# Optimization experiments

Hardware: AMD Instinct MI355X
Metric: run time of the kernel (lower is better)

Reference implementation:

```python
import jax, jax.numpy as jnp
import numpy as np

EPS = 1e-12  # F.normalize default eps


def _unfold(x, k, pad, stride):
    # torch F.unfold: [B,C,H,W] -> [B, C*k*k, L], features ordered (c, kh, kw), L row-major.
    B, C, H, W = x.shape
    xp = jnp.pad(x, ((0, 0), (0, 0), (pad, pad), (pad, pad)))
    Ho = (H + 2 * pad - k) // stride + 1
    Wo = (W + 2 * pad - k) // stride + 1
    r = (jnp.arange(Ho) * stride)[:, None] + jnp.arange(k)[None, :]  # [Ho,k]
    c = (jnp.arange(Wo) * stride)[:, None] + jnp.arange(k)[None, :]  # [Wo,k]
    p = xp[:, :, r[:, None, :, None], c[None, :, None, :]]  # [B,C,Ho,Wo,k,k]
    return p.transpose(0, 1, 4, 5, 2, 3).reshape(B, C * k * k, Ho * Wo)


def _fold(p, out_hw, k, pad, stride):
    # torch F.fold: overlap-add inverse of _unfold.
    B, CKK, L = p.shape
    C = CKK // (k * k)
    H, W = out_hw
    Ho = (H + 2 * pad - k) // stride + 1
    Wo = (W + 2 * pad - k) // stride + 1
    p = p.reshape(B, C, k, k, Ho, Wo).transpose(0, 1, 4, 5, 2, 3)  # [B,C,Ho,Wo,k,k]
    r = (jnp.arange(Ho) * stride)[:, None] + jnp.arange(k)[None, :]
    c = (jnp.arange(Wo) * stride)[:, None] + jnp.arange(k)[None, :]
    out = jnp.zeros((B, C, H + 2 * pad, W + 2 * pad), p.dtype)
    out = out.at[:, :, r[:, None, :, None], c[None, :, None, :]].add(p)
    return out[:, :, pad:pad + H, pad:pad + W]


def _l2n(x, axis):
    n = jnp.sqrt(jnp.sum(x * x, axis=axis, keepdims=True))
    return x / jnp.maximum(n, EPS)


def setup_inputs() -> dict:
    key = jax.random.key(0)
    ks = jax.random.split(key, 11)
    B, H, W = 1, 32, 32
    f = jnp.float32
    return {
        'lrsr_lv3': jax.random.normal(ks[0], (B, 256, H, W), f),
        'refsr_lv1': jax.random.normal(ks[1], (B, 64, 4 * H, 4 * W), f),
        'refsr_lv2': jax.random.normal(ks[2], (B, 128, 2 * H, 2 * W), f),
        'refsr_lv3': jax.random.normal(ks[3], (B, 256, H, W), f),
        'ref_lv1': jax.random.normal(ks[4], (B, 64, 4 * H, 4 * W), f),
        'ref_lv2': jax.random.normal(ks[5], (B, 128, 2 * H, 2 * W), f),
        'ref_lv3': jax.random.normal(ks[6], (B, 256, H, W), f),
        'W1': jax.random.normal(ks[7], (2304, 1152), f) * 0.02,
        'b1': jax.random.normal(ks[8], (2304,), f) * 0.02,
        'W2': jax.random.normal(ks[9], (2304, 576), f) * 0.02,
        'b2': jax.random.normal(ks[10], (2304,), f) * 0.02,
    }


def reference(lrsr_lv3, refsr_lv1, refsr_lv2, refsr_lv3, ref_lv1, ref_lv2, ref_lv3, W1, b1, W2, b2):
    B, _, H, W = lrsr_lv3.shape
    lr3 = _unfold(lrsr_lv3, 3, 1, 1)                       # [B, 2304, N]
    r3 = _unfold(refsr_lv3, 3, 1, 1).transpose(0, 2, 1)    # [B, N3, 2304]
    r2 = _unfold(refsr_lv2, 3, 1, 1).transpose(0, 2, 1) @ W1.T + b1  # [B, N2, 2304]
    r1 = _unfold(refsr_lv1, 3, 1, 1).transpose(0, 2, 1) @ W2.T + b2  # [B, N1, 2304]
    r3 = _l2n(r3, 2); r2 = _l2n(r2, 2); r1 = _l2n(r1, 2)
    lr3 = _l2n(lr3, 1)
    R3 = jnp.einsum('bnd,bdm->bnm', r3, lr3)  # [B, N3, N]
    R2 = jnp.einsum('bnd,bdm->bnm', r2, lr3)  # [B, N2, N]
    R1 = jnp.einsum('bnd,bdm->bnm', r1, lr3)  # [B, N1, N]
    R3_star = jnp.max(R3, axis=1); R3_arg = jnp.argmax(R3, axis=1)
    R2_star = jnp.max(R2, axis=1)
    R1_star = jnp.max(R1, axis=1)
    ref3u = _unfold(ref_lv3, 3, 1, 1)
    ref2u = _unfold(ref_lv2, 6, 2, 2)
    ref1u = _unfold(ref_lv1, 12, 4, 4)
    idx = R3_arg[:, None, :]  # [B,1,N] broadcast over feature dim
    T3u = jnp.take_along_axis(ref3u, idx, axis=2)
    T2u = jnp.take_along_axis(ref2u, idx, axis=2)
    T1u = jnp.take_along_axis(ref1u, idx, axis=2)
    T_lv3 = _fold(T3u, (H, W), 3, 1, 1) / 9.0
    T_lv2 = _fold(T2u, (2 * H, 2 * W), 6, 2, 2) / 9.0
    T_lv1 = _fold(T1u, (4 * H, 4 * W), 12, 4, 4) / 9.0
    S_3 = R3_star.reshape(B, 1, H, W)
    S_2 = R2_star.reshape(B, 1, H, W)
    S_1 = R1_star.reshape(B, 1, H, W)
    return (S_1, S_2, S_3, T_lv3, T_lv2, T_lv1)
```

## Files before the change

### kernel.cpp

```cpp
#include <hip/hip_runtime.h>

typedef short bf8 __attribute__((ext_vector_type(8)));
typedef float f32x4 __attribute__((ext_vector_type(4)));

static __device__ __forceinline__ unsigned short f2bf(float f) {
  unsigned u = __float_as_uint(f);
  unsigned r = u + 0x7FFFu + ((u >> 16) & 1u);
  return (unsigned short)(r >> 16);
}
static __device__ __forceinline__ float bf2f(unsigned short h) {
  return __uint_as_float(((unsigned)h) << 16);
}
static __device__ __forceinline__ unsigned fkey(float f) {
  unsigned u = __float_as_uint(f);
  return (u & 0x80000000u) ? ~u : (u | 0x80000000u);
}
static __device__ __forceinline__ float kdec(unsigned k) {
  unsigned u = (k & 0x80000000u) ? (k & 0x7FFFFFFFu) : ~k;
  return __uint_as_float(u);
}
static __device__ __forceinline__ int xcdswz(int h, int nwg) {
  int q = nwg >> 3, r = nwg & 7;
  int xcd = h & 7, w = h >> 3;
  return (xcd < r ? xcd * (q + 1) : r * (q + 1) + (xcd - r) * q) + w;
}
static __device__ __forceinline__ int xcdbal(int h, int nwg, int nb0) {
  int xcd = h & 7, w = h >> 3;
  int qa = nb0 >> 3, qb = (nwg - nb0) >> 3;
  return (w < qa) ? (xcd * qa + w) : (nb0 + xcd * qb + (w - qa));
}

static __device__ __forceinline__ void gload_lds16(const unsigned short* g, unsigned short* l) {
  __builtin_amdgcn_global_load_lds((const __attribute__((address_space(1))) void*)g,
                                   (__attribute__((address_space(3))) void*)l, 16, 0, 0);
}

static __device__ __forceinline__ float uf3(const float* __restrict__ src, int lgS, int d, int m) {
  const int S = 1 << lgS;
  int cc = d / 9;
  int r9 = d - cc * 9;
  int ki = r9 / 3;
  int kj = r9 - ki * 3;
  int i = (m >> lgS) + ki - 1;
  int j = (m & (S - 1)) + kj - 1;
  if ((unsigned)i >= (unsigned)S || (unsigned)j >= (unsigned)S) return 0.f;
  return src[((size_t)cc << (2 * lgS)) + ((size_t)i << lgS) + j];
}

__global__ __launch_bounds__(256) void k_prepA(const float* __restrict__ lrsr3, const float* __restrict__ rsr3,
                                               const float* __restrict__ rsr2, const float* __restrict__ rsr1,
                                               const float* __restrict__ W1, const float* __restrict__ W2,
                                               const float* __restrict__ b1, const float* __restrict__ b2,
                                               float* __restrict__ sclr, float* __restrict__ scu3,
                                               float* __restrict__ bl2, float* __restrict__ bl1,
                                               float* __restrict__ G2,
                                               float* __restrict__ rsr2t, float* __restrict__ rsr1t,
                                               unsigned short* __restrict__ lr3nbT,
                                               unsigned short* __restrict__ W1t, unsigned short* __restrict__ W2t) {
  const int blk = blockIdx.x;
  const int tid = threadIdx.x;
  if (blk < 2048) {
    __shared__ float r0[256], r1[256], r2[256];
    const bool lr = blk < 1024;
    const int m = blk & 1023;
    const float* src = lr ? lrsr3 : rsr3;
    float s = 0.f, d1 = 0.f, d2 = 0.f;
    for (int d = tid; d < 2304; d += 256) {
      float v = uf3(src, 5, d, m);
      s += v * v; d1 += b1[d] * v; d2 += b2[d] * v;
    }
    r0[tid] = s; r1[tid] = d1; r2[tid] = d2;
    __syncthreads();
    for (int o = 128; o > 0; o >>= 1) {
      if (tid < o) { r0[tid] += r0[tid + o]; r1[tid] += r1[tid + o]; r2[tid] += r2[tid + o]; }
      __syncthreads();
    }
    if (tid == 0) {
      float sc = 1.f / fmaxf(sqrtf(r0[0]), 1e-12f);
      if (lr) { sclr[m] = sc; bl2[m] = r1[0] * sc; bl1[m] = r2[0] * sc; }
      else    { scu3[m] = sc; }
    }
  } else if (blk < 3072) {
    __shared__ float As[16][32], Bs[16][32];
    const int px = blk - 2048;
    const int m0 = (px >> 5) * 32, n0 = (px & 31) * 32;
    const int tx = tid & 15, ty = tid >> 4;
    float acc[2][2] = {};
    for (int kb = 0; kb < 256; kb += 16) {
      __syncthreads();
      {
        int kk = tid >> 5, mm = tid & 31;
        As[kk][mm] = lrsr3[(size_t)(kb + kk) * 1024 + m0 + mm];
        Bs[kk][mm] = rsr3[(size_t)(kb + kk) * 1024 + n0 + mm];
        int e2 = tid + 256; int kk2 = e2 >> 5, mm2 = e2 & 31;
        As[kk2][mm2] = lrsr3[(size_t)(kb + kk2) * 1024 + m0 + mm2];
        Bs[kk2][mm2] = rsr3[(size_t)(kb + kk2) * 1024 + n0 + mm2];
      }
      __syncthreads();
#pragma unroll
      for (int kk = 0; kk < 16; ++kk) {
        float a0 = As[kk][ty * 2], a1 = As[kk][ty * 2 + 1];
        float b0 = Bs[kk][tx * 2], b1v = Bs[kk][tx * 2 + 1];
        acc[0][0] = fmaf(a0, b0, acc[0][0]); acc[0][1] = fmaf(a0, b1v, acc[0][1]);
        acc[1][0] = fmaf(a1, b0, acc[1][0]); acc[1][1] = fmaf(a1, b1v, acc[1][1]);
      }
    }
#pragma unroll
    for (int i = 0; i < 2; ++i)
#pragma unroll
      for (int jj = 0; jj < 2; ++jj)
        G2[(size_t)(m0 + ty * 2 + i) * 1024 + (n0 + tx * 2 + jj)] = acc[i][jj];
  } else if (blk < 3200) {
    __shared__ float Tt[64][65];
    const int idx = blk - 3072;
    const int ct = idx & 1, st = idx >> 1;
#pragma unroll
    for (int i = 0; i < 16; ++i) {
      int id = tid + i * 256;
      int r = id >> 6, c = id & 63;
      Tt[r][c] = rsr2[(size_t)(ct * 64 + r) * 4096 + st * 64 + c];
    }
    __syncthreads();
#pragma unroll
    for (int i = 0; i < 16; ++i) {
      int id = tid + i * 256;
      int cc2 = id >> 6, rr = id & 63;
      rsr2t[(size_t)(st * 64 + cc2) * 128 + ct * 64 + rr] = Tt[rr][cc2];
    }
  } else if (blk < 3456) {
    __shared__ float Tt[64][65];
    const int st = blk - 3200;
#pragma unroll
    for (int i = 0; i < 16; ++i) {
      int id = tid + i * 256;
      int r = id >> 6, c = id & 63;
      Tt[r][c] = rsr1[(size_t)r * 16384 + st * 64 + c];
    }
    __syncthreads();
#pragma unroll
    for (int i = 0; i < 16; ++i) {
      int id = tid + i * 256;
      int cc2 = id >> 6, rr = id & 63;
      rsr1t[(size_t)(st * 64 + cc2) * 64 + rr] = Tt[rr][cc2];
    }
  } else if (blk < 4608) {
    int id8 = (blk - 3456) * 256 + tid;
    int m = id8 / 288, c0 = (id8 - m * 288) * 8;
    bf8 v;
#pragma unroll
    for (int e = 0; e < 8; ++e) v[e] = (short)f2bf(uf3(lrsr3, 5, c0 + e, m));
    *(bf8*)(lr3nbT + (size_t)m * 2304 + c0) = v;
  } else {
    __shared__ unsigned short Ls[64][65];
    int idx = blk - 4608;
    int xx = idx % 27, yy = idx / 27;
    const float* W; unsigned short* Wt; int Cw, c0;
    if (xx < 18) { W = W1; Wt = W1t; Cw = 1152; c0 = xx * 64; }
    else         { W = W2; Wt = W2t; Cw = 576;  c0 = (xx - 18) * 64; }
    const int Cch = Cw / 9;
    const int d0 = yy * 64;
#pragma unroll
    for (int i = 0; i < 16; ++i) {
      int id = tid + i * 256;
      int r = id >> 6, c = id & 63;
      Ls[r][c] = f2bf(W[(size_t)(d0 + r) * Cw + c0 + c]);
    }
    __syncthreads();
#pragma unroll
    for (int i = 0; i < 16; ++i) {
      int id = tid + i * 256;
      int cc = id >> 6, rr = id & 63;
      int c = c0 + cc;
      Wt[(size_t)((c % 9) * Cch + c / 9) * 2304 + d0 + rr] = Ls[rr][cc];
    }
  }
}

struct Job {
  const unsigned short* Alo;
  const unsigned short* Ahi;
  const unsigned short* Bt;
  unsigned short* Clo;
  unsigned short* Chi;
  const float* bl;
  const float* bw;
  const float* bbp;
  const float* rowscale;
  float* pnsq;
  float* pbwd;
  float* cmax;
  int Msplit, N, K, nbx, Mtot, npart, which;
};

template <int EPI, int NBUF>
static __device__ __forceinline__ void gemm_body(const Job& j0, const Job& j1, int nb0, int bid) {
  __shared__ __align__(16) unsigned short As[NBUF][128 * 64];
  __shared__ __align__(16) unsigned short Bs[NBUF][128 * 64];
  __shared__ unsigned colkey[128];
  __shared__ float ninvL[128];

  const bool first = (bid < nb0);
  const Job j = first ? j0 : j1;
  const int local = bid - (first ? 0 : nb0);
  const int by = local / j.nbx;
  const int bx = local - by * j.nbx;
  const int m0 = by * 128, n0 = bx * 128;
  const int K = j.K, N = j.N;

  const unsigned short* Abase = (m0 < j.Msplit)
      ? j.Alo + (size_t)m0 * K
      : j.Ahi + (size_t)(m0 - j.Msplit) * K;

  const int tid = threadIdx.x;
  const int l = tid & 63;
  const int w = tid >> 6;
  const int wr = w >> 1, wc = w & 1;
  if (EPI == 2) {
    if (tid < 128) {
      colkey[tid] = 0u;
      const int r = m0 + tid;
      float nsq = 0.f, bwd = 0.f;
      for (int p = 0; p < j.npart; ++p) {
        nsq += j.pnsq[(size_t)p * j.Mtot + r];
        bwd += j.pbwd[(size_t)p * j.Mtot + r];
      }
      float tq = nsq + 2.f * bwd + j.bbp[j.which];
      ninvL[tid] = 1.f / fmaxf(sqrtf(fmaxf(tq, 0.f)), 1e-12f);
    }
  }

  f32x4 acc[4][4] = {};

  const int srow = w * 32;
  const int lrow = l >> 3;
  const int gcol = ((l & 7) ^ lrow) * 8;
  const int mr = l & 15;
  const int kg = l >> 4;

  const int nt = K >> 6;
  const int snap_kb = n0 + wc * 64;
  unsigned short snap[4][4][4];

  auto stage = [&](int buf, int kb) {
#pragma unroll
    for (int i = 0; i < 4; ++i) {
      int r = srow + i * 8;
      gload_lds16(Abase + (size_t)(r + lrow) * K + kb + gcol, &As[buf][r * 64]);
      gload_lds16(j.Bt + (size_t)(n0 + r + lrow) * K + kb + gcol, &Bs[buf][r * 64]);
    }
  };
  auto compute_tile = [&](int cur) {
#pragma unroll
    for (int ks = 0; ks < 2; ++ks) {
      bf8 af[4], bv[4];
#pragma unroll
      for (int mi = 0; mi < 4; ++mi) {
        const int row = wr * 64 + mi * 16 + mr;
        af[mi] = *(const bf8*)&As[cur][row * 64 + (((ks * 4 + kg) ^ (row & 7)) * 8)];
      }
#pragma unroll
      for (int ni = 0; ni < 4; ++ni) {
        const int row = wc * 64 + ni * 16 + mr;
        bv[ni] = *(const bf8*)&Bs[cur][row * 64 + (((ks * 4 + kg) ^ (row & 7)) * 8)];
      }
      __builtin_amdgcn_s_setprio(1);
#pragma unroll
      for (int mi = 0; mi < 4; ++mi)
#pragma unroll
        for (int ni = 0; ni < 4; ++ni)
          acc[mi][ni] = __builtin_amdgcn_mfma_f32_16x16x32_bf16(af[mi], bv[ni], acc[mi][ni], 0, 0, 0);
      __builtin_amdgcn_s_setprio(0);
    }
  };
  auto do_snap = [&](int cur) {
#pragma unroll
    for (int mi = 0; mi < 4; ++mi)
#pragma unroll
      for (int e = 0; e < 4; ++e) {
        const int row = wr * 64 + mi * 16 + kg * 4 + e;
#pragma unroll
        for (int ni = 0; ni < 4; ++ni) {
          const int slot = ni * 2 + (mr >> 3);
          snap[mi][ni][e] = As[cur][row * 64 + ((slot ^ (row & 7)) * 8) + (mr & 7)];
        }
      }
  };

  if constexpr (NBUF == 1) {
    for (int t = 0; t < nt; ++t) {
      if (t) __syncthreads();
      stage(0, t << 6);
      __syncthreads();
      compute_tile(0);
      if (EPI == 1 && (t << 6) == snap_kb) do_snap(0);
    }
  } else {
    auto waitv = [&](int Wt) {
      if (Wt >= 2)      asm volatile("s_waitcnt vmcnt(16)\ns_barrier" ::: "memory");
      else if (Wt == 1) asm volatile("s_waitcnt vmcnt(8)\ns_barrier" ::: "memory");
      else              asm volatile("s_waitcnt vmcnt(0)\ns_barrier" ::: "memory");
    };
#pragma unroll
    for (int p = 0; p < NBUF; ++p) if (p < nt) stage(p, p << 6);
    { int inflight = (NBUF < nt ? NBUF : nt); waitv(inflight - 1); }
    int cur = 0;
    for (int t = 0; t < nt; ++t) {
      compute_tile(cur);
      if (EPI == 1 && (t << 6) == snap_kb) do_snap(cur);
      if (t + 1 < nt) {
        asm volatile("s_waitcnt lgkmcnt(0)\ns_barrier" ::: "memory");
        if (t + NBUF < nt) stage(cur, (t + NBUF) << 6);
        const int im = (nt - 1 < t + NBUF) ? (nt - 1) : (t + NBUF);
        waitv(im - (t + 1));
        cur = (cur + 1 == NBUF) ? 0 : cur + 1;
      }
    }
  }

  const int lr0 = wr * 64;
  const int lc0 = wc * 64;
  if (EPI == 0) {
    const bool hi = (m0 >= j.Msplit);
    unsigned short* Cbase = hi ? j.Chi + (size_t)(m0 - j.Msplit) * N
                               : j.Clo + (size_t)m0 * N;
    float rs[4][4];
#pragma unroll
    for (int mi = 0; mi < 4; ++mi)
#pragma unroll
      for (int e = 0; e < 4; ++e)
        rs[mi][e] = hi ? j.rowscale[m0 - j.Msplit + lr0 + mi * 16 + kg * 4 + e] : 1.f;
#pragma unroll
    for (int mi = 0; mi < 4; ++mi)
#pragma unroll
      for (int ni = 0; ni < 4; ++ni)
#pragma unroll
        for (int e = 0; e < 4; ++e)
          Cbase[(size_t)(lr0 + mi * 16 + kg * 4 + e) * (size_t)N + (n0 + lc0 + ni * 16 + mr)] =
              f2bf(acc[mi][ni][e] * rs[mi][e]);
  } else if (EPI == 1) {
    float rp[4][4] = {};
    float bp[4][4] = {};
#pragma unroll
    for (int ni = 0; ni < 4; ++ni) {
      const float bwv = j.bw[n0 + lc0 + ni * 16 + mr];
#pragma unroll
      for (int mi = 0; mi < 4; ++mi)
#pragma unroll
        for (int e = 0; e < 4; ++e) {
          const float av = bf2f(snap[mi][ni][e]);
          rp[mi][e] += acc[mi][ni][e] * av;
          bp[mi][e] += bwv * av;
        }
    }
#pragma unroll
    for (int off = 1; off < 16; off <<= 1)
#pragma unroll
      for (int mi = 0; mi < 4; ++mi)
#pragma unroll
        for (int e = 0; e < 4; ++e) {
          rp[mi][e] += __shfl_xor(rp[mi][e], off);
          bp[mi][e] += __shfl_xor(bp[mi][e], off);
        }
    if (mr == 0) {
      const size_t slotbase = (size_t)(bx * 2 + wc) * j.Mtot;
#pragma unroll
      for (int mi = 0; mi < 4; ++mi)
#pragma unroll
        for (int e = 0; e < 4; ++e) {
          const int r = m0 + lr0 + mi * 16 + kg * 4 + e;
          j.pnsq[slotbase + r] = rp[mi][e];
          j.pbwd[slotbase + r] = bp[mi][e];
        }
    }
  } else {
    float nv[4][4];
#pragma unroll
    for (int mi = 0; mi < 4; ++mi)
#pragma unroll
      for (int e = 0; e < 4; ++e)
        nv[mi][e] = ninvL[lr0 + mi * 16 + kg * 4 + e];
#pragma unroll
    for (int ni = 0; ni < 4; ++ni) {
      float blv = j.bl[n0 + lc0 + ni * 16 + mr];
      float mx = -3.0e38f;
#pragma unroll
      for (int mi = 0; mi < 4; ++mi)
#pragma unroll
        for (int e = 0; e < 4; ++e) mx = fmaxf(mx, (acc[mi][ni][e] + blv) * nv[mi][e]);
      atomicMax(&colkey[lc0 + ni * 16 + mr], fkey(mx));
    }
    __syncthreads();
    if (tid < 128) j.cmax[(size_t)by * 1024 + n0 + tid] = kdec(colkey[tid]);
  }
}

__global__ __launch_bounds__(256) void k_prepBP(Job pa, Job pb, int nbP0,
                                                const float* __restrict__ rsr2t, const float* __restrict__ rsr1t,
                                                const float* __restrict__ W1, const float* __restrict__ W2,
                                                const float* __restrict__ b1, const float* __restrict__ b2,
                                                const float* __restrict__ sclr, const float* __restrict__ scu3,
                                                const float* __restrict__ G2,
                                                unsigned short* __restrict__ U2b, unsigned short* __restrict__ U1b,
                                                float* __restrict__ bw2, float* __restrict__ bw1,
                                                float* __restrict__ bb,
                                                float* __restrict__ s3, int* __restrict__ arg) {
  const int blk = blockIdx.x;
  const int tid = threadIdx.x;
  if (blk < 218) {
    gemm_body<0, 1>(pa, pb, nbP0, xcdswz(blk, 218));
  } else if (blk < 2522) {
    int id = (blk - 218) * 256 + tid;
    int t = id & 15, rest = id >> 4;
    int kk = rest % 9, n = rest / 9;
    int cc0 = t * 8;
    int ki = kk / 3, kj = kk - ki * 3;
    int sy = (n >> 6) + ki - 1, sx = (n & 63) + kj - 1;
    bf8 v;
    if ((unsigned)sy < 64u && (unsigned)sx < 64u) {
      const float* p = rsr2t + (size_t)(sy * 64 + sx) * 128 + cc0;
      f32x4 a = *(const f32x4*)p;
      f32x4 bq = *(const f32x4*)(p + 4);
#pragma unroll
      for (int e = 0; e < 4; ++e) { v[e] = (short)f2bf(a[e]); v[4 + e] = (short)f2bf(bq[e]); }
    } else {
#pragma unroll
      for (int e = 0; e < 8; ++e) v[e] = 0;
    }
    *(bf8*)(U2b + (size_t)n * 1152 + kk * 128 + cc0) = v;
  } else if (blk < 7642) {
    int id = (blk - 2522) * 256 + tid;
    int n = id / 80, rem = id - n * 80;
    int ks = rem >> 3, t = rem & 7;
    int cc0 = t * 8;
    bf8 v;
    if (ks == 9) {
#pragma unroll
      for (int e = 0; e < 8; ++e) v[e] = 0;
    } else {
      int ki = ks / 3, kj = ks - ki * 3;
      int sy = (n >> 7) + ki - 1, sx = (n & 127) + kj - 1;
      if ((unsigned)sy < 128u && (unsigned)sx < 128u) {
        const float* p = rsr1t + (size_t)(sy * 128 + sx) * 64 + cc0;
        f32x4 a = *(const f32x4*)p;
        f32x4 bq = *(const f32x4*)(p + 4);
#pragma unroll
        for (int e = 0; e < 4; ++e) { v[e] = (short)f2bf(a[e]); v[4 + e] = (short)f2bf(bq[e]); }
      } else {
#pragma unroll
        for (int e = 0; e < 8; ++e) v[e] = 0;
      }
    }
    *(bf8*)(U1b + (size_t)n * 640 + ks * 64 + cc0) = v;
  } else if (blk < 7722) {
    __shared__ float red[256];
    int idx = blk - 7642;
    int x = idx & 7, y = idx >> 3;
    if (y == 9) {
      if (x >= 2) return;
      const float* b = x ? b2 : b1;
      float s = 0.f;
      for (int d = tid; d < 2304; d += 256) s += b[d] * b[d];
      red[tid] = s; __syncthreads();
      for (int o = 128; o > 0; o >>= 1) { if (tid < o) red[tid] += red[tid + o]; __syncthreads(); }
      if (tid == 0) bb[x] = red[0];
      return;
    }
    const bool two = x < 5;
    const float* W = two ? W1 : W2;
    const float* b = two ? b1 : b2;
    float* bw = two ? bw2 : bw1;
    const int Cw = two ? 1152 : 576;
    int c = (two ? x : x - 5) * 256 + tid;
    if (c >= Cw) return;
    int d0 = y * 256;
    float s = 0.f;
    for (int d = d0; d < d0 + 256; ++d) s += b[d] * W[(size_t)d * Cw + c];
    atomicAdd(&bw[(c % 9) * (Cw / 9) + c / 9], s);
  } else {
    __shared__ float bv[256]; __shared__ int bidx[256];
    const int m = blk - 7722;
    const int mi = m >> 5, mj = m & 31;
    float best = -3.0e38f; int bi = 0;
    for (int n = tid; n < 1024; n += 256) {
      const int ni = n >> 5, nj = n & 31;
      float raw = 0.f;
#pragma unroll
      for (int dy = -1; dy <= 1; ++dy) {
#pragma unroll
        for (int dx = -1; dx <= 1; ++dx) {
          bool vm = ((unsigned)(mi + dy) < 32u) && ((unsigned)(mj + dx) < 32u);
          bool vn = ((unsigned)(ni + dy) < 32u) && ((unsigned)(nj + dx) < 32u);
          if (vm && vn) {
            int off = dy * 32 + dx;
            raw += G2[(size_t)(m + off) * 1024 + (n + off)];
          }
        }
      }
      float v = raw * scu3[n];
      if (v > best) { best = v; bi = n; }
    }
    bv[tid] = best; bidx[tid] = bi;
    __syncthreads();
    for (int o = 128; o > 0; o >>= 1) {
      if (tid < o) {
        float ov = bv[tid + o]; int oi = bidx[tid + o];
        if (ov > bv[tid] || (ov == bv[tid] && oi < bidx[tid])) { bv[tid] = ov; bidx[tid] = oi; }
      }
      __syncthreads();
    }
    if (tid == 0) { s3[m] = bv[0] * sclr[m]; arg[m] = bidx[0]; }
  }
}

__global__ __launch_bounds__(256) void k_gE1(Job a, Job b, int nb0) {
  gemm_body<1, 1>(a, b, nb0, xcdbal((int)blockIdx.x, (int)gridDim.x, nb0));
}
__global__ __launch_bounds__(256) void k_gE2(Job a, Job b, int nb0) {
  gemm_body<2, 1>(a, b, nb0, xcdbal((int)blockIdx.x, (int)gridDim.x, nb0));
}

__global__ __launch_bounds__(256) void k_tfold(const float* __restrict__ ref3, const float* __restrict__ ref2,
                                               const float* __restrict__ ref1, const int* __restrict__ arg,
                                               const float* __restrict__ cmax1, const float* __restrict__ cmax2,
                                               float* __restrict__ out) {
  const int bid = blockIdx.x;
  const int tid = threadIdx.x;
  if (bid < 256) {
    __shared__ float plane[1024];
    __shared__ int argL[1024];
    const int c = bid;
#pragma unroll
    for (int k = 0; k < 4; ++k) {
      plane[k * 256 + tid] = ref3[(size_t)c * 1024 + k * 256 + tid];
      argL[k * 256 + tid] = arg[k * 256 + tid];
    }
    __syncthreads();
#pragma unroll
    for (int k = 0; k < 4; ++k) {
      int px = k * 256 + tid;
      int y = px >> 5, x = px & 31;
      float s = 0.f;
#pragma unroll
      for (int di = -1; di <= 1; ++di) {
        int i = y + di;
        if ((unsigned)i >= 32u) continue;
#pragma unroll
        for (int dj = -1; dj <= 1; ++dj) {
          int jw = x + dj;
          if ((unsigned)jw >= 32u) continue;
          int n2 = argL[i * 32 + jw];
          int rr = (n2 >> 5) + y - i, cc = (n2 & 31) + x - jw;
          if ((unsigned)rr < 32u && (unsigned)cc < 32u) s += plane[rr * 32 + cc];
        }
      }
      out[3072 + (size_t)c * 1024 + px] = s * (1.f / 9.f);
    }
  } else if (bid < 1280) {
    __shared__ int argL[1024];
#pragma unroll
    for (int k = 0; k < 4; ++k) argL[k * 256 + tid] = arg[k * 256 + tid];
    __syncthreads();
    int id2 = (bid - 256) * 256 + tid;
    int q = id2 & 31, y = (id2 >> 5) & 63, c = id2 >> 11;
    int iy = y >> 1;
    float s0 = 0.f, s1 = 0.f;
#pragma unroll
    for (int di = -1; di <= 1; ++di) {
      int i = iy + di;
      if ((unsigned)i >= 32u) continue;
      int ry = y - 2 * i;
#pragma unroll
      for (int dj = -1; dj <= 1; ++dj) {
        int jw = q + dj;
        if ((unsigned)jw >= 32u) continue;
        int n2 = argL[i * 32 + jw];
        int rr = (n2 >> 5) * 2 + ry;
        int cb = (n2 & 31) * 2 + 2 * (q - jw);
        if ((unsigned)rr < 64u && (unsigned)cb < 63u) {
          const float* p = ref2 + (size_t)c * 4096 + rr * 64 + cb;
          s0 += p[0]; s1 += p[1];
        }
      }
    }
    float2 o; o.x = s0 * (1.f / 9.f); o.y = s1 * (1.f / 9.f);
    *(float2*)(out + 265216 + (size_t)c * 4096 + y * 64 + 2 * q) = o;
  } else if (bid < 2304) {
    __shared__ int argL[1024];
#pragma unroll
    for (int k = 0; k < 4; ++k) argL[k * 256 + tid] = arg[k * 256 + tid];
    __syncthreads();
    int id1 = (bid - 1280) * 256 + tid;
    int q = id1 & 31, y = (id1 >> 5) & 127, c = id1 >> 12;
    int iy = y >> 2;
    f32x4 s = {0.f, 0.f, 0.f, 0.f};
#pragma unroll
    for (int di = -1; di <= 1; ++di) {
      int i = iy + di;
      if ((unsigned)i >= 32u) continue;
      int ry = y - 4 * i;
#pragma unroll
      for (int dj = -1; dj <= 1; ++dj) {
        int jw = q + dj;
        if ((unsigned)jw >= 32u) continue;
        int n2 = argL[i * 32 + jw];
        int rr = (n2 >> 5) * 4 + ry;
        int cb = (n2 & 31) * 4 + 4 * (q - jw);
        if ((unsigned)rr < 128u && (unsigned)cb < 125u) {
          f32x4 v = *(const f32x4*)(ref1 + (size_t)c * 16384 + rr * 128 + cb);
          s += v;
        }
      }
    }
    s *= (1.f / 9.f);
    *(f32x4*)(out + 789504 + (size_t)c * 16384 + y * 128 + 4 * q) = s;
  } else {
    int t = (bid - 2304) * 256 + tid;
    if (t < 1024) {
      float mx = -3.0e38f;
      for (int rb = 0; rb < 128; ++rb) mx = fmaxf(mx, cmax1[rb * 1024 + t]);
      out[t] = mx;
    } else {
      int tt = t - 1024;
      float mx = -3.0e38f;
      for (int rb = 0; rb < 32; ++rb) mx = fmaxf(mx, cmax2[rb * 1024 + tt]);
      out[1024 + tt] = mx;
    }
  }
}

static constexpr size_t OFF_BW2     = 0;
static constexpr size_t OFF_BW1     = 4608;
static constexpr size_t ZERO_BYTES  = 7168;
static constexpr size_t OFF_BB      = 7168;
static constexpr size_t OFF_BL2     = 7424;
static constexpr size_t OFF_BL1     = 11520;
static constexpr size_t OFF_SCLR    = 15616;
static constexpr size_t OFF_SCU3    = 19712;
static constexpr size_t OFF_R3ARG   = 23808;
static constexpr size_t OFF_PNSQ2   = 27904;
static constexpr size_t OFF_PBWD2   = OFF_PNSQ2 + 294912;
static constexpr size_t OFF_PNSQ1   = OFF_PBWD2 + 294912;
static constexpr size_t OFF_PBWD1   = OFF_PNSQ1 + 655360;
static constexpr size_t OFF_CMAX2   = OFF_PBWD1 + 655360;
static constexpr size_t OFF_CMAX1   = OFF_CMAX2 + 131072;
static constexpr size_t OFF_LR3NBT  = OFF_CMAX1 + 524288;
static constexpr size_t OFF_U2B     = OFF_LR3NBT + 4718592;
static constexpr size_t OFF_U1B     = OFF_U2B    + 9437184;
static constexpr size_t OFF_W1T     = OFF_U1B    + 20971520;
static constexpr size_t OFF_W2T     = OFF_W1T    + 5308416;
static constexpr size_t OFF_A2      = OFF_W2T    + 2949120;
static constexpr size_t OFF_A1      = OFF_A2     + 2654208;
static constexpr size_t OFF_M2T     = OFF_A1     + 819200;
static constexpr size_t OFF_M1T     = OFF_M2T    + 2359296;
static constexpr size_t OFF_G2      = OFF_M1T    + 1310720;
static constexpr size_t OFF_R2T     = OFF_G2     + 4194304;
static constexpr size_t OFF_R1T     = OFF_R2T    + 2097152;

extern "C" void kernel_launch(void* const* d_in, const int* in_sizes, int n_in,
                              void* d_out, int out_size, void* d_ws, size_t ws_size,
                              hipStream_t stream) {
  (void)in_sizes; (void)n_in; (void)out_size; (void)ws_size;
  const float* lrsr3  = (const float*)d_in[0];
  const float* rsr1   = (const float*)d_in[1];
  const float* rsr2   = (const float*)d_in[2];
  const float* rsr3   = (const float*)d_in[3];
  const float* ref1   = (const float*)d_in[4];
  const float* ref2   = (const float*)d_in[5];
  const float* ref3   = (const float*)d_in[6];
  const float* W1     = (const float*)d_in[7];
  const float* b1     = (const float*)d_in[8];
  const float* W2     = (const float*)d_in[9];
  const float* b2     = (const float*)d_in[10];
  float* out = (float*)d_out;
  char* ws = (char*)d_ws;

  float*          bw2     = (float*)(ws + OFF_BW2);
  float*          bw1     = (float*)(ws + OFF_BW1);
  float*          bb      = (float*)(ws + OFF_BB);
  float*          bl2     = (float*)(ws + OFF_BL2);
  float*          bl1     = (float*)(ws + OFF_BL1);
  float*          sclr    = (float*)(ws + OFF_SCLR);
  float*          scu3    = (float*)(ws + OFF_SCU3);
  int*            R3arg   = (int*)(ws + OFF_R3ARG);
  float*          pnsq2   = (float*)(ws + OFF_PNSQ2);
  float*          pbwd2   = (float*)(ws + OFF_PBWD2);
  float*          pnsq1   = (float*)(ws + OFF_PNSQ1);
  float*          pbwd1   = (float*)(ws + OFF_PBWD1);
  float*          cmax2   = (float*)(ws + OFF_CMAX2);
  float*          cmax1   = (float*)(ws + OFF_CMAX1);
  unsigned short* lr3nbT  = (unsigned short*)(ws + OFF_LR3NBT);
  unsigned short* U2b     = (unsigned short*)(ws + OFF_U2B);
  unsigned short* U1b     = (unsigned short*)(ws + OFF_U1B);
  unsigned short* W1t     = (unsigned short*)(ws + OFF_W1T);
  unsigned short* W2t     = (unsigned short*)(ws + OFF_W2T);
  unsigned short* A2b     = (unsigned short*)(ws + OFF_A2);
  unsigned short* A1b     = (unsigned short*)(ws + OFF_A1);
  unsigned short* M2tb    = (unsigned short*)(ws + OFF_M2T);
  unsigned short* M1tb    = (unsigned short*)(ws + OFF_M1T);
  float*          G2      = (float*)(ws + OFF_G2);
  float*          rsr2t   = (float*)(ws + OFF_R2T);
  float*          rsr1t   = (float*)(ws + OFF_R1T);

  hipMemsetAsync(d_ws, 0, ZERO_BYTES, stream);
  hipMemsetAsync(ws + OFF_W2T + (size_t)576 * 2304 * 2, 0, (size_t)64 * 2304 * 2, stream);

  k_prepA<<<5580, 256, 0, stream>>>(lrsr3, rsr3, rsr2, rsr1, W1, W2, b1, b2,
                                    sclr, scu3, bl2, bl1, G2, rsr2t, rsr1t, lr3nbT, W1t, W2t);

  Job jz = {};
  {
    Job a = jz, b = jz;
    a.Alo = W1t; a.Ahi = lr3nbT; a.Msplit = 1152; a.Bt = W1t;
    a.Clo = A2b; a.Chi = M2tb; a.rowscale = sclr; a.N = 1152; a.K = 2304; a.nbx = 9;
    b.Alo = W2t; b.Ahi = lr3nbT; b.Msplit = 640; b.Bt = W2t;
    b.Clo = A1b; b.Chi = M1tb; b.rowscale = sclr; b.N = 640; b.K = 2304; b.nbx = 5;
    k_prepBP<<<8746, 256, 0, stream>>>(a, b, 153, rsr2t, rsr1t, W1, W2, b1, b2, sclr, scu3, G2,
                                       U2b, U1b, bw2, bw1, bb, out + 2048, R3arg);
  }
  {
    Job a = jz, b = jz;
    a.Alo = U2b; a.Ahi = U2b; a.Msplit = 4096; a.Bt = A2b;
    a.bw = bw2; a.pnsq = pnsq2; a.pbwd = pbwd2; a.Mtot = 4096;
    a.N = 1152; a.K = 1152; a.nbx = 9;
    b.Alo = U1b; b.Ahi = U1b; b.Msplit = 16384; b.Bt = A1b;
    b.bw = bw1; b.pnsq = pnsq1; b.pbwd = pbwd1; b.Mtot = 16384;
    b.N = 640; b.K = 640; b.nbx = 5;
    k_gE1<<<288 + 640, 256, 0, stream>>>(a, b, 288);
  }
  {
    Job a = jz, b = jz;
    a.Alo = U2b; a.Ahi = U2b; a.Msplit = 4096; a.Bt = M2tb;
    a.bl = bl2; a.pnsq = pnsq2; a.pbwd = pbwd2; a.bbp = bb;
    a.npart = 18; a.which = 0; a.cmax = cmax2; a.Mtot = 4096;
    a.N = 1024; a.K = 1152; a.nbx = 8;
    b.Alo = U1b; b.Ahi = U1b; b.Msplit = 16384; b.Bt = M1tb;
    b.bl = bl1; b.pnsq = pnsq1; b.pbwd = pbwd1; b.bbp = bb;
    b.npart = 10; b.which = 1; b.cmax = cmax1; b.Mtot = 16384;
    b.N = 1024; b.K = 640; b.nbx = 8;
    k_gE2<<<256 + 1024, 256, 0, stream>>>(a, b, 256);
  }

  k_tfold<<<2312, 256, 0, stream>>>(ref3, ref2, ref1, R3arg, cmax1, cmax2, out);
}
```

Measured before the change: 207.9 us.

## Replace per-patch norm/bias-dot blocks with per-pixel channel sums plus 3x3 window

```diff
diff --git a/kernel.cpp b/kernel.cpp
--- a/kernel.cpp
+++ b/kernel.cpp
@@ -28,6 +28,23 @@
   int xcd = h & 7, w = h >> 3;
   int qa = nb0 >> 3, qb = (nwg - nb0) >> 3;
   return (w < qa) ? (xcd * qa + w) : (nb0 + xcd * qb + (w - qa));
+}
+static __device__ __forceinline__ float win9s(const float* __restrict__ b, int m) {
+  int mi = m >> 5, mj = m & 31;
+  float s = 0.f;
+#pragma unroll
+  for (int dy = -1; dy <= 1; ++dy) {
+    int i = mi + dy; if ((unsigned)i >= 32u) continue;
+#pragma unroll
+    for (int dx = -1; dx <= 1; ++dx) {
+      int jx = mj + dx; if ((unsigned)jx >= 32u) continue;
+      s += b[i * 32 + jx];
+    }
+  }
+  return s;
+}
+static __device__ __forceinline__ float rswin(const float* __restrict__ b, int m) {
+  return 1.f / fmaxf(sqrtf(win9s(b, m)), 1e-12f);
 }
 
 static __device__ __forceinline__ void gload_lds16(const unsigned short* g, unsigned short* l) {
@@ -51,38 +68,46 @@
                                                const float* __restrict__ rsr2, const float* __restrict__ rsr1,
                                                const float* __restrict__ W1, const float* __restrict__ W2,
                                                const float* __restrict__ b1, const float* __restrict__ b2,
-                                               float* __restrict__ sclr, float* __restrict__ scu3,
-                                               float* __restrict__ bl2, float* __restrict__ bl1,
                                                float* __restrict__ G2,
                                                float* __restrict__ rsr2t, float* __restrict__ rsr1t,
                                                unsigned short* __restrict__ lr3nbT,
-                                               unsigned short* __restrict__ W1t, unsigned short* __restrict__ W2t) {
+                                               unsigned short* __restrict__ W1t, unsigned short* __restrict__ W2t,
+                                               float* __restrict__ ssumL, float* __restrict__ ssumR,
+                                               float* __restrict__ D1, float* __restrict__ D2) {
   const int blk = blockIdx.x;
   const int tid = threadIdx.x;
-  if (blk < 2048) {
-    __shared__ float r0[256], r1[256], r2[256];
-    const bool lr = blk < 1024;
-    const int m = blk & 1023;
-    const float* src = lr ? lrsr3 : rsr3;
-    float s = 0.f, d1 = 0.f, d2 = 0.f;
-    for (int d = tid; d < 2304; d += 256) {
-      float v = uf3(src, 5, d, m);
-      s += v * v; d1 += b1[d] * v; d2 += b2[d] * v;
-    }
-    r0[tid] = s; r1[tid] = d1; r2[tid] = d2;
-    __syncthreads();
-    for (int o = 128; o > 0; o >>= 1) {
-      if (tid < o) { r0[tid] += r0[tid + o]; r1[tid] += r1[tid + o]; r2[tid] += r2[tid + o]; }
+  if (blk < 8) {
+    const bool lr = blk < 4;
+    const int p = (blk & 3) * 256 + tid;
+    if (lr) {
+      __shared__ float b1L[2304], b2L[2304];
+      for (int i = tid; i < 2304; i += 256) { b1L[i] = b1[i]; b2L[i] = b2[i]; }
       __syncthreads();
-    }
-    if (tid == 0) {
-      float sc = 1.f / fmaxf(sqrtf(r0[0]), 1e-12f);
-      if (lr) { sclr[m] = sc; bl2[m] = r1[0] * sc; bl1[m] = r2[0] * sc; }
-      else    { scu3[m] = sc; }
-    }
-  } else if (blk < 3072) {
+      float ss = 0.f;
+      float d1a[9] = {}, d2a[9] = {};
+      for (int cc = 0; cc < 256; ++cc) {
+        float v = lrsr3[(size_t)cc * 1024 + p];
+        ss = fmaf(v, v, ss);
+#pragma unroll
+        for (int kk = 0; kk < 9; ++kk) {
+          d1a[kk] = fmaf(b1L[cc * 9 + kk], v, d1a[kk]);
+          d2a[kk] = fmaf(b2L[cc * 9 + kk], v, d2a[kk]);
+        }
+      }
+      ssumL[p] = ss;
+#pragma unroll
+      for (int kk = 0; kk < 9; ++kk) { D1[kk * 1024 + p] = d1a[kk]; D2[kk * 1024 + p] = d2a[kk]; }
+    } else {
+      float ss = 0.f;
+      for (int cc = 0; cc < 256; ++cc) {
+        float v = rsr3[(size_t)cc * 1024 + p];
+        ss = fmaf(v, v, ss);
+      }
+      ssumR[p] = ss;
+    }
+  } else if (blk < 1032) {
     __shared__ float As[16][32], Bs[16][32];
-    const int px = blk - 2048;
+    const int px = blk - 8;
     const int m0 = (px >> 5) * 32, n0 = (px & 31) * 32;
     const int tx = tid & 15, ty = tid >> 4;
     float acc[2][2] = {};
@@ -110,9 +135,9 @@
 #pragma unroll
       for (int jj = 0; jj < 2; ++jj)
         G2[(size_t)(m0 + ty * 2 + i) * 1024 + (n0 + tx * 2 + jj)] = acc[i][jj];
-  } else if (blk < 3200) {
+  } else if (blk < 1160) {
     __shared__ float Tt[64][65];
-    const int idx = blk - 3072;
+    const int idx = blk - 1032;
     const int ct = idx & 1, st = idx >> 1;
 #pragma unroll
     for (int i = 0; i < 16; ++i) {
@@ -127,9 +152,9 @@
       int cc2 = id >> 6, rr = id & 63;
       rsr2t[(size_t)(st * 64 + cc2) * 128 + ct * 64 + rr] = Tt[rr][cc2];
     }
-  } else if (blk < 3456) {
+  } else if (blk < 1416) {
     __shared__ float Tt[64][65];
-    const int st = blk - 3200;
+    const int st = blk - 1160;
 #pragma unroll
     for (int i = 0; i < 16; ++i) {
       int id = tid + i * 256;
@@ -143,8 +168,8 @@
       int cc2 = id >> 6, rr = id & 63;
       rsr1t[(size_t)(st * 64 + cc2) * 64 + rr] = Tt[rr][cc2];
     }
-  } else if (blk < 4608) {
-    int id8 = (blk - 3456) * 256 + tid;
+  } else if (blk < 2568) {
+    int id8 = (blk - 1416) * 256 + tid;
     int m = id8 / 288, c0 = (id8 - m * 288) * 8;
     bf8 v;
 #pragma unroll
@@ -152,7 +177,7 @@
     *(bf8*)(lr3nbT + (size_t)m * 2304 + c0) = v;
   } else {
     __shared__ unsigned short Ls[64][65];
-    int idx = blk - 4608;
+    int idx = blk - 2568;
     int xx = idx % 27, yy = idx / 27;
     const float* W; unsigned short* Wt; int Cw, c0;
     if (xx < 18) { W = W1; Wt = W1t; Cw = 1152; c0 = xx * 64; }
@@ -185,7 +210,7 @@
   const float* bl;
   const float* bw;
   const float* bbp;
-  const float* rowscale;
+  const float* rowss;
   float* pnsq;
   float* pbwd;
   float* cmax;
@@ -328,7 +353,7 @@
     for (int mi = 0; mi < 4; ++mi)
 #pragma unroll
       for (int e = 0; e < 4; ++e)
-        rs[mi][e] = hi ? j.rowscale[m0 - j.Msplit + lr0 + mi * 16 + kg * 4 + e] : 1.f;
+        rs[mi][e] = hi ? rswin(j.rowss, m0 - j.Msplit + lr0 + mi * 16 + kg * 4 + e) : 1.f;
 #pragma unroll
     for (int mi = 0; mi < 4; ++mi)
 #pragma unroll
@@ -398,11 +423,13 @@
                                                 const float* __restrict__ rsr2t, const float* __restrict__ rsr1t,
                                                 const float* __restrict__ W1, const float* __restrict__ W2,
                                                 const float* __restrict__ b1, const float* __restrict__ b2,
-                                                const float* __restrict__ sclr, const float* __restrict__ scu3,
+                                                const float* __restrict__ ssumL, const float* __restrict__ ssumR,
+                                                const float* __restrict__ D1, const float* __restrict__ D2,
                                                 const float* __restrict__ G2,
                                                 unsigned short* __restrict__ U2b, unsigned short* __restrict__ U1b,
                                                 float* __restrict__ bw2, float* __restrict__ bw1,
                                                 float* __restrict__ bb,
+                                                float* __restrict__ bl2, float* __restrict__ bl1,
                                                 float* __restrict__ s3, int* __restrict__ arg) {
   const int blk = blockIdx.x;
   const int tid = threadIdx.x;
@@ -476,7 +503,7 @@
     float s = 0.f;
     for (int d = d0; d < d0 + 256; ++d) s += b[d] * W[(size_t)d * Cw + c];
     atomicAdd(&bw[(c % 9) * (Cw / 9) + c / 9], s);
-  } else {
+  } else if (blk < 8746) {
     __shared__ float bv[256]; __shared__ int bidx[256];
     const int m = blk - 7722;
     const int mi = m >> 5, mj = m & 31;
@@ -496,7 +523,7 @@
           }
         }
       }
-      float v = raw * scu3[n];
+      float v = raw * rswin(ssumR, n);
       if (v > best) { best = v; bi = n; }
     }
     bv[tid] = best; bidx[tid] = bi;
@@ -508,7 +535,27 @@
       }
       __syncthreads();
     }
-    if (tid == 0) { s3[m] = bv[0] * sclr[m]; arg[m] = bidx[0]; }
+    if (tid == 0) { s3[m] = bv[0] * rswin(ssumL, m); arg[m] = bidx[0]; }
+  } else {
+    int m = (blk - 8746) * 256 + tid;
+    int mi = m >> 5, mj = m & 31;
+    float s = 0.f, a1 = 0.f, a2 = 0.f;
+#pragma unroll
+    for (int ki = 0; ki < 3; ++ki) {
+      int i = mi + ki - 1; if ((unsigned)i >= 32u) continue;
+#pragma unroll
+      for (int kj = 0; kj < 3; ++kj) {
+        int jx = mj + kj - 1; if ((unsigned)jx >= 32u) continue;
+        int pix = i * 32 + jx;
+        int kk = ki * 3 + kj;
+        s += ssumL[pix];
+        a1 += D1[kk * 1024 + pix];
+        a2 += D2[kk * 1024 + pix];
+      }
+    }
+    float sc = 1.f / fmaxf(sqrtf(s), 1e-12f);
+    bl2[m] = a1 * sc;
+    bl1[m] = a2 * sc;
   }
 }
 
@@ -634,8 +681,8 @@
 static constexpr size_t OFF_BB      = 7168;
 static constexpr size_t OFF_BL2     = 7424;
 static constexpr size_t OFF_BL1     = 11520;
-static constexpr size_t OFF_SCLR    = 15616;
-static constexpr size_t OFF_SCU3    = 19712;
+static constexpr size_t OFF_SSUML   = 15616;
+static constexpr size_t OFF_SSUMR   = 19712;
 static constexpr size_t OFF_R3ARG   = 23808;
 static constexpr size_t OFF_PNSQ2   = 27904;
 static constexpr size_t OFF_PBWD2   = OFF_PNSQ2 + 294912;
@@ -655,6 +702,8 @@
 static constexpr size_t OFF_G2      = OFF_M1T    + 1310720;
 static constexpr size_t OFF_R2T     = OFF_G2     + 4194304;
 static constexpr size_t OFF_R1T     = OFF_R2T    + 2097152;
+static constexpr size_t OFF_D1      = OFF_R1T    + 4194304;
+static constexpr size_t OFF_D2      = OFF_D1     + 36864;
 
 extern "C" void kernel_launch(void* const* d_in, const int* in_sizes, int n_in,
                               void* d_out, int out_size, void* d_ws, size_t ws_size,
@@ -679,8 +728,8 @@
   float*          bb      = (float*)(ws + OFF_BB);
   float*          bl2     = (float*)(ws + OFF_BL2);
   float*          bl1     = (float*)(ws + OFF_BL1);
-  float*          sclr    = (float*)(ws + OFF_SCLR);
-  float*          scu3    = (float*)(ws + OFF_SCU3);
+  float*          ssumL   = (float*)(ws + OFF_SSUML);
+  float*          ssumR   = (float*)(ws + OFF_SSUMR);
   int*            R3arg   = (int*)(ws + OFF_R3ARG);
   float*          pnsq2   = (float*)(ws + OFF_PNSQ2);
   float*          pbwd2   = (float*)(ws + OFF_PBWD2);
@@ -700,22 +749,25 @@
   float*          G2      = (float*)(ws + OFF_G2);
   float*          rsr2t   = (float*)(ws + OFF_R2T);
   float*          rsr1t   = (float*)(ws + OFF_R1T);
+  float*          D1      = (float*)(ws + OFF_D1);
+  float*          D2      = (float*)(ws + OFF_D2);
 
   hipMemsetAsync(d_ws, 0, ZERO_BYTES, stream);
   hipMemsetAsync(ws + OFF_W2T + (size_t)576 * 2304 * 2, 0, (size_t)64 * 2304 * 2, stream);
 
-  k_prepA<<<5580, 256, 0, stream>>>(lrsr3, rsr3, rsr2, rsr1, W1, W2, b1, b2,
-                                    sclr, scu3, bl2, bl1, G2, rsr2t, rsr1t, lr3nbT, W1t, W2t);
+  k_prepA<<<3540, 256, 0, stream>>>(lrsr3, rsr3, rsr2, rsr1, W1, W2, b1, b2,
+                                    G2, rsr2t, rsr1t, lr3nbT, W1t, W2t, ssumL, ssumR, D1, D2);
 
   Job jz = {};
   {
     Job a = jz, b = jz;
     a.Alo = W1t; a.Ahi = lr3nbT; a.Msplit = 1152; a.Bt = W1t;
-    a.Clo = A2b; a.Chi = M2tb; a.rowscale = sclr; a.N = 1152; a.K = 2304; a.nbx = 9;
+    a.Clo = A2b; a.Chi = M2tb; a.rowss = ssumL; a.N = 1152; a.K = 2304; a.nbx = 9;
     b.Alo = W2t; b.Ahi = lr3nbT; b.Msplit = 640; b.Bt = W2t;
-    b.Clo = A1b; b.Chi = M1tb; b.rowscale = sclr; b.N = 640; b.K = 2304; b.nbx = 5;
-    k_prepBP<<<8746, 256, 0, stream>>>(a, b, 153, rsr2t, rsr1t, W1, W2, b1, b2, sclr, scu3, G2,
-                                       U2b, U1b, bw2, bw1, bb, out + 2048, R3arg);
+    b.Clo = A1b; b.Chi = M1tb; b.rowss = ssumL; b.N = 640; b.K = 2304; b.nbx = 5;
+    k_prepBP<<<8750, 256, 0, stream>>>(a, b, 153, rsr2t, rsr1t, W1, W2, b1, b2,
+                                       ssumL, ssumR, D1, D2, G2,
+                                       U2b, U1b, bw2, bw1, bb, bl2, bl1, out + 2048, R3arg);
   }
   {
     Job a = jz, b = jz;
```

After: 220.4 us. 1.06x slower.
